# Optimization experiments

Hardware: AMD Instinct MI355X
Metric: run time of the kernel (lower is better)

The kernel has to match this reference:

```python
import jax, jax.numpy as jnp
import numpy as np

ITERATIONS = 7


def _arnold_indices(n):
    # tf.meshgrid(range(width), range(height)) -> x[i,j]=j, y[i,j]=i (shape [H,W])
    x, y = jnp.meshgrid(jnp.arange(n), jnp.arange(n))
    new_x = (2 * x + y) % n
    new_y = (x + y) % n
    # tf.transpose(tf.stack([new_y,new_x],0)) reverses dims [2,H,W] -> [W,H,2],
    # so indices[i,j] = (new_y[j,i], new_x[j,i])
    return new_y.T, new_x.T


def setup_inputs() -> dict:
    key = jax.random.key(0)
    inputs = jax.random.normal(key, (16, 1024, 1024, 3), dtype=jnp.float32)
    return {"inputs": inputs}


def reference(inputs) -> jnp.ndarray:
    n = inputs.shape[1]  # square images: H == W
    iy, ix = _arnold_indices(n)  # same map every iteration
    for _ in range(ITERATIONS):
        # out[b,i,j,c] = inputs[b, iy[i,j], ix[i,j], c]  (gather_nd + map_fn, vectorized over batch)
        inputs = inputs[:, iy, ix, :]
    return inputs
```

## Files before the change

kernel.cpp:

```cpp
#include <hip/hip_runtime.h>


#define N_DIM 1024
#define MASKN 1023
#define TR 64
#define TC 64
#define LPITCH (TR * 3 + 1)

__global__ __launch_bounds__(256) void arnold_cat7_kernel(
    const float* __restrict__ in, float* __restrict__ out) {
    __shared__ float lds[TC * LPITCH];

    const int tile = blockIdx.x;
    const int b    = blockIdx.y;
    const int r0   = (tile >> 4) * TR;
    const int c0   = (tile & 15) * TC;
    const int t    = threadIdx.x;

    const size_t img = (size_t)b * (size_t)(N_DIM * N_DIM * 3);
    const float* __restrict__ inb  = in + img;
    float* __restrict__ outb       = out + img;

#pragma unroll
    for (int k = 0; k < 16; ++k) {
        const int q       = t + 256 * k;
        const int c_local = q >> 6;
        const int dr      = q & 63;
        const int c       = c0 + c_local;
        const int R       = (169 * c) & MASKN;
        const int col     = (r0 + dr + 239 * c) & MASKN;
        const float* __restrict__ src = inb + ((size_t)R * N_DIM + (size_t)col) * 3;
        float* dst = &lds[c_local * LPITCH + dr * 3];
        dst[0] = src[0];
        dst[1] = src[1];
        dst[2] = src[2];
    }

    __syncthreads();

#pragma unroll
    for (int k = 0; k < 16; ++k) {
        const int q       = t + 256 * k;
        const int r_local = q >> 6;
        const int dc      = q & 63;
        const int r       = r0 + r_local;
        const int i       = (169 * r) & MASKN;
        const int j       = (c0 + dc + 41 * i) & MASKN;
        float* __restrict__ dst = outb + ((size_t)i * N_DIM + (size_t)j) * 3;
        const float* src = &lds[dc * LPITCH + r_local * 3];
        dst[0] = src[0];
        dst[1] = src[1];
        dst[2] = src[2];
    }
}

extern "C" void kernel_launch(void* const* d_in, const int* in_sizes, int n_in,
                              void* d_out, int out_size, void* d_ws, size_t ws_size,
                              hipStream_t stream) {
    (void)in_sizes; (void)n_in; (void)d_ws; (void)ws_size; (void)out_size;
    const float* in = (const float*)d_in[0];
    float* out      = (float*)d_out;
    dim3 grid(256, 16, 1);
    dim3 block(256, 1, 1);
    hipLaunchKernelGGL(arnold_cat7_kernel, grid, block, 0, stream, in, out);
}
```

Measured before the change: 338.6 us.

## Remap tiles across XCDs and use 512-thread blocks with 32-bit addressing

Flattens the grid to 1D and remaps block IDs so that consecutive row strips are spread over the eight XCDs, while blocks on the same XCD share the same strip. The goal is better L2 locality for the gathered input rows. Blocks grow from 256 to 512 threads, so each thread does 8 iterations instead of 16. Pointer offsets are now computed in 32-bit unsigned arithmetic to make address generation cheaper. The remap depends on the hardware scheduling blocks round-robin across XCDs.

```diff
diff --git a/kernel.cpp b/kernel.cpp
--- a/kernel.cpp
+++ b/kernel.cpp
@@ -1,56 +1,56 @@
 #include <hip/hip_runtime.h>
 
 
-#define N_DIM 1024
-#define MASKN 1023
-#define TR 64
-#define TC 64
-#define LPITCH (TR * 3 + 1)
+#define NDIM    1024
+#define MASKN   1023
+#define LPITCHF 193
 
-__global__ __launch_bounds__(256) void arnold_cat7_kernel(
+__global__ __launch_bounds__(512) void arnold_cat7_kernel(
     const float* __restrict__ in, float* __restrict__ out) {
-    __shared__ float lds[TC * LPITCH];
+    __shared__ float lds[64 * LPITCHF];
 
-    const int tile = blockIdx.x;
-    const int b    = blockIdx.y;
-    const int r0   = (tile >> 4) * TR;
-    const int c0   = (tile & 15) * TC;
-    const int t    = threadIdx.x;
+    const int B     = blockIdx.x;
+    const int xcd   = B & 7;
+    const int q     = B >> 3;
+    const int c0i   = q & 15;
+    const int strip = ((q >> 4) << 3) | xcd;
+    const int bimg  = strip >> 4;
+    const int r0    = (strip & 15) << 6;
+    const int c0    = c0i << 6;
 
-    const size_t img = (size_t)b * (size_t)(N_DIM * N_DIM * 3);
-    const float* __restrict__ inb  = in + img;
-    float* __restrict__ outb       = out + img;
+    const int t  = threadIdx.x;
+    const int w  = t >> 6;
+    const int dr = t & 63;
+
+    const float* __restrict__ inb = in  + (size_t)bimg * (size_t)(NDIM * NDIM * 3);
+    float* __restrict__ outb      = out + (size_t)bimg * (size_t)(NDIM * NDIM * 3);
 
 #pragma unroll
-    for (int k = 0; k < 16; ++k) {
-        const int q       = t + 256 * k;
-        const int c_local = q >> 6;
-        const int dr      = q & 63;
-        const int c       = c0 + c_local;
-        const int R       = (169 * c) & MASKN;
-        const int col     = (r0 + dr + 239 * c) & MASKN;
-        const float* __restrict__ src = inb + ((size_t)R * N_DIM + (size_t)col) * 3;
-        float* dst = &lds[c_local * LPITCH + dr * 3];
+    for (int k = 0; k < 8; ++k) {
+        const int c_local = w + 8 * k;
+        const int c   = c0 + c_local;
+        const int R   = (169 * c) & MASKN;
+        const int col = (r0 + dr + 239 * c) & MASKN;
+        const float* __restrict__ src = inb + (unsigned)(R * NDIM + col) * 3u;
+        float* __restrict__ dst = &lds[c_local * LPITCHF + dr * 3];
         dst[0] = src[0];
         dst[1] = src[1];
         dst[2] = src[2];
     }
-
     __syncthreads();
 
 #pragma unroll
-    for (int k = 0; k < 16; ++k) {
-        const int q       = t + 256 * k;
-        const int r_local = q >> 6;
-        const int dc      = q & 63;
-        const int r       = r0 + r_local;
-        const int i       = (169 * r) & MASKN;
-        const int j       = (c0 + dc + 41 * i) & MASKN;
-        float* __restrict__ dst = outb + ((size_t)i * N_DIM + (size_t)j) * 3;
-        const float* src = &lds[dc * LPITCH + r_local * 3];
-        dst[0] = src[0];
-        dst[1] = src[1];
-        dst[2] = src[2];
+    for (int k = 0; k < 8; ++k) {
+        const int r_local = w + 8 * k;
+        const int dc = dr;
+        const int r  = r0 + r_local;
+        const int i  = (169 * r) & MASKN;
+        const int j  = (c0 + dc + 41 * i) & MASKN;
+        const float* __restrict__ s = &lds[dc * LPITCHF + r_local * 3];
+        float* __restrict__ d = outb + (unsigned)(i * NDIM + j) * 3u;
+        d[0] = s[0];
+        d[1] = s[1];
+        d[2] = s[2];
     }
 }
 
@@ -60,7 +60,7 @@
     (void)in_sizes; (void)n_in; (void)d_ws; (void)ws_size; (void)out_size;
     const float* in = (const float*)d_in[0];
     float* out      = (float*)d_out;
-    dim3 grid(256, 16, 1);
-    dim3 block(256, 1, 1);
+    dim3 grid(4096, 1, 1);
+    dim3 block(512, 1, 1);
     hipLaunchKernelGGL(arnold_cat7_kernel, grid, block, 0, stream, in, out);
 }
```

Result: no change. 332.8 us (-1.7%).
